# Kernel tuning notes

Hardware: AMD Instinct MI355X
Metric: run time of the kernel (lower is better)

## Reference

```python
import jax, jax.numpy as jnp
import numpy as np

# Straight-through sign binarization: forward -> {-1, +1}, backward -> identity
@jax.custom_vjp
def binarize(x):
    return jnp.where(x >= 0, jnp.ones_like(x), -jnp.ones_like(x))

def _bin_fwd(x):
    return binarize(x), None

def _bin_bwd(res, g):
    return (g,)

binarize.defvjp(_bin_fwd, _bin_bwd)

BATCH = 16384
IN_SIZE = 1025   # must be 2**n + 1
HIDDEN = 1025    # must be 2**n + 1

def setup_inputs() -> dict:
    key = jax.random.key(0)
    k0, k1, k2, k3 = jax.random.split(key, 4)
    # weight init scale per reset_parameters: sqrt(1.5/(in+out)) uniform
    s = float(np.sqrt(1.5 / (IN_SIZE + HIDDEN)))
    return {
        "x": jax.random.normal(k0, (BATCH, IN_SIZE), dtype=jnp.float32),
        "W0": jax.random.uniform(k1, (HIDDEN, IN_SIZE), jnp.float32, -s, s),
        "W1": jax.random.uniform(k2, (HIDDEN, HIDDEN), jnp.float32, -s, s),
        "W2": jax.random.uniform(k3, (1, HIDDEN), jnp.float32, -s, s),
    }

def reference(x, W0, W1, W2):
    # x: [B, IN_SIZE]; weights stored [out, in] (nn.Linear convention), no bias
    h = x.reshape(-1, IN_SIZE)
    for W in (W0, W1, W2):
        lin = h @ binarize(W).T          # float GEMM against +/-1 weights
        h = binarize(lin)                # sign activation
    # num_classes == 2 path: to_boolean maps {-1,+1} -> {0,1}, then squeeze
    out = (h + 1.0) * 0.5
    return out.squeeze(-1)               # [B]
```

## Files before the change

### kernel.cpp

```cpp
#include <hip/hip_runtime.h>
#include <cstdint>

typedef unsigned long long u64;
typedef unsigned short ushort_t;
typedef __attribute__((ext_vector_type(8))) short short8;
typedef __attribute__((ext_vector_type(4))) float f32x4;

#define B_TOTAL 16384
#define K_DIM   1025
#define O_DIM   1025
#define NWORDS  17
#define NKT     34
#define NFRAG   72
#define A_BYTES 8192
#define B_BYTES 73728
#define SMEM_BYTES 99328
#define FLAG_CAP 4096
#define L23_ROWS 16

__device__ __forceinline__ ushort_t f2bf_rne(float f) {
  unsigned u = __float_as_uint(f);
  return (ushort_t)((u + 0x7fffu + ((u >> 16) & 1u)) >> 16);
}

__global__ __launch_bounds__(256) void pack_all_kernel(const float* __restrict__ W0,
                                                       const float* __restrict__ W1,
                                                       const float* __restrict__ W2,
                                                       u64* __restrict__ w0b,
                                                       u64* __restrict__ w1b,
                                                       u64* __restrict__ w2b) {
  __shared__ unsigned char by[136];
  const int row = blockIdx.x, t = threadIdx.x;
  const float* src; u64* dst; int o;
  if (row < O_DIM)           { src = W0; dst = w0b; o = row; }
  else if (row < 2 * O_DIM)  { src = W1; dst = w1b; o = row - O_DIM; }
  else                       { src = W2; dst = w2b; o = 0; }
  if (t < 136) {
    const float* wr = src + (size_t)o * K_DIM;
    unsigned m = 0;
#pragma unroll
    for (int j = 0; j < 8; ++j) {
      int k = t * 8 + j;
      bool pos = (k < K_DIM) ? (wr[k] >= 0.0f) : true;
      m |= (unsigned)pos << j;
    }
    by[t] = (unsigned char)m;
  }
  __syncthreads();
  if (t < NWORDS) {
    u64 word = 0;
#pragma unroll
    for (int q = 0; q < 8; ++q) word |= (u64)by[t * 8 + q] << (8 * q);
    dst[(size_t)o * NWORDS + t] = word;
  }
}

__global__ __launch_bounds__(256) void prep_sbf_kernel(const float* __restrict__ w0,
                                                       ushort_t* __restrict__ sbf) {
  const int t = threadIdx.x;
  const int f = blockIdx.x * 4 + (t >> 6);
  const int lane = t & 63;
  const int kt = f / NFRAG, nf = f % NFRAG;
  const int o = nf * 16 + (lane & 15);
  const int kbase = kt * 32 + (lane >> 4) * 8;
  short8 sv;
#pragma unroll
  for (int j = 0; j < 8; ++j) {
    int k = kbase + j;
    short v = 0;
    if (o < O_DIM && k < K_DIM)
      v = (short)((w0[(size_t)o * K_DIM + k] >= 0.0f) ? 0x3F80 : 0xBF80);
    sv[j] = v;
  }
  *(short8*)&sbf[(size_t)f * 512 + lane * 8] = sv;
}

__global__ __launch_bounds__(512, 1) void l1_fused_kernel(
    const ushort_t* __restrict__ sbf, const float* __restrict__ x,
    const u64* __restrict__ w0b, u64* __restrict__ h1b) {
  extern __shared__ char smem[];
  const int p = blockIdx.x;
  const int t = threadIdx.x;
  const int wave = t >> 6, lane = t & 63;
  const int lr = lane & 15, lg = lane >> 4;
  const int b0 = p * 64;
  const int obase = wave * 144;

  const int u = t & 255;
  const int cmf = u >> 6, clane = u & 63;
  const int crow = cmf * 16 + (clane & 15);
  const int ckb0 = (clane >> 4) * 8;
  const bool isLo = (t >= 256);
  const float* xrowC = x + (size_t)(b0 + crow) * K_DIM;
  const int convOff = (isLo ? 4096 : 0) + cmf * 1024 + clane * 16;

  const ushort_t* gB = sbf + (size_t)(wave * 9) * 512 + lane * 8;

  f32x4 acc[4][9];
#pragma unroll
  for (int mf = 0; mf < 4; ++mf)
#pragma unroll
    for (int nfl = 0; nfl < 9; ++nfl)
#pragma unroll
      for (int c = 0; c < 4; ++c) acc[mf][nfl][c] = 0.0f;

  float xv[8];
  float sAcc = 0.0f;
  short8 bX[9];

#define LOADX(KT)                                                              \
  {                                                                            \
    int kb = (KT) * 32 + ckb0;                                                 \
    const float* xr = xrowC + kb;                                              \
    if (kb + 8 <= K_DIM) {                                                     \
      float4 a = *(const float4*)xr;                                           \
      float4 b = *(const float4*)(xr + 4);                                     \
      xv[0]=a.x; xv[1]=a.y; xv[2]=a.z; xv[3]=a.w;                              \
      xv[4]=b.x; xv[5]=b.y; xv[6]=b.z; xv[7]=b.w;                              \
    } else {                                                                   \
      _Pragma("unroll")                                                        \
      for (int j = 0; j < 8; ++j) xv[j] = (kb + j < K_DIM) ? xr[j] : 0.0f;     \
    }                                                                          \
  }

#define CONVERT_WRITE(DBUF)                                                    \
  {                                                                            \
    short8 w8;                                                                 \
    if (!isLo) {                                                               \
      _Pragma("unroll")                                                        \
      for (int j = 0; j < 8; ++j) {                                            \
        float v = xv[j];                                                       \
        sAcc += fabsf(v);                                                      \
        w8[j] = (short)f2bf_rne(v);                                            \
      }                                                                        \
    } else {                                                                   \
      _Pragma("unroll")                                                        \
      for (int j = 0; j < 8; ++j) {                                            \
        float v = xv[j];                                                       \
        ushort_t h = f2bf_rne(v);                                              \
        float hf = __uint_as_float((unsigned)h << 16);                         \
        w8[j] = (short)f2bf_rne(v - hf);                                       \
      }                                                                        \
    }                                                                          \
    *(short8*)((DBUF) + convOff) = w8;                                         \
  }

#define LOADB(KT)                                                              \
  {                                                                            \
    _Pragma("unroll")                                                          \
    for (int i = 0; i < 9; ++i)                                                \
      bX[i] = *(const short8*)&gB[(size_t)(KT) * (B_BYTES / 2) + i * 512];     \
  }

#define MFMA_STEP(AOFF, KTN)                                                   \
  {                                                                            \
    const ushort_t* A = (const ushort_t*)(smem + (AOFF));                      \
    const ushort_t* gBn = gB + (size_t)(KTN) * (B_BYTES / 2);                  \
    short8 ah[4], al[4];                                                       \
    _Pragma("unroll")                                                          \
    for (int mf = 0; mf < 4; ++mf) {                                           \
      ah[mf] = *(const short8*)&A[mf * 512 + lane * 8];                        \
      al[mf] = *(const short8*)&A[(4 + mf) * 512 + lane * 8];                  \
    }                                                                          \
    _Pragma("unroll")                                                          \
    for (int nfl = 0; nfl < 9; ++nfl) {                                        \
      short8 bv = bX[nfl];                                                     \
      bX[nfl] = *(const short8*)&gBn[nfl * 512];                               \
      _Pragma("unroll")                                                        \
      for (int mf = 0; mf < 4; ++mf) {                                         \
        acc[mf][nfl] = __builtin_amdgcn_mfma_f32_16x16x32_bf16(ah[mf], bv, acc[mf][nfl], 0, 0, 0); \
        acc[mf][nfl] = __builtin_amdgcn_mfma_f32_16x16x32_bf16(al[mf], bv, acc[mf][nfl], 0, 0, 0); \
      }                                                                        \
    }                                                                          \
  }

#define LDS_BARRIER()                                                          \
  {                                                                            \
    asm volatile("s_waitcnt lgkmcnt(0)" ::: "memory");                         \
    __builtin_amdgcn_s_barrier();                                              \
  }

  LOADX(0); CONVERT_WRITE(smem);
  LOADB(0);
  LOADX(1);
  LDS_BARRIER();

  for (int kt = 0; kt < NKT; kt += 2) {
    {
      CONVERT_WRITE(smem + 8192);
      if (kt + 2 < NKT) LOADX(kt + 2);
      MFMA_STEP(0, kt + 1);
      LDS_BARRIER();
    }
    {
      if (kt + 2 < NKT) CONVERT_WRITE(smem);
      if (kt + 3 < NKT) LOADX(kt + 3);
      const int ktn = (kt + 2 < NKT) ? (kt + 2) : (NKT - 1);
      MFMA_STEP(8192, ktn);
      LDS_BARRIER();
    }
  }
#undef LOADX
#undef CONVERT_WRITE
#undef LOADB
#undef MFMA_STEP
#undef LDS_BARRIER

  __syncthreads();

  unsigned char* bits = (unsigned char*)smem;
  u64*      hs    = (u64*)(smem + 73728);
  unsigned* list  = (unsigned*)(smem + 82432);
  unsigned* lcnt  = (unsigned*)(smem + 98816);
  float*    errbL = (float*)(smem + 98832);
  unsigned* hsw   = (unsigned*)hs;

  sAcc += __shfl_xor(sAcc, 16, 64);
  sAcc += __shfl_xor(sAcc, 32, 64);
  if (t == 0) *lcnt = 0;
  if (!isLo && lg == 0)
    errbL[crow] = sAcc * (1.02f / 65536.0f) + 0.125f;
  __syncthreads();

  float eb[4][4];
#pragma unroll
  for (int mf = 0; mf < 4; ++mf)
#pragma unroll
    for (int rg = 0; rg < 4; ++rg) eb[mf][rg] = errbL[mf * 16 + lg * 4 + rg];

#pragma unroll
  for (int mf = 0; mf < 4; ++mf)
#pragma unroll
    for (int nfl = 0; nfl < 9; ++nfl)
#pragma unroll
      for (int rg = 0; rg < 4; ++rg) {
        int bl = mf * 16 + lg * 4 + rg;
        int o  = obase + nfl * 16 + lr;
        float lin = acc[mf][nfl][rg];
        unsigned abit = (lin >= 0.0f) ? 1u : 0u;
        bits[bl * 1152 + o] = (unsigned char)abit;
        if ((o < O_DIM) && (fabsf(lin) <= eb[mf][rg])) {
          unsigned idx = atomicAdd(lcnt, 1u);
          if (idx < FLAG_CAP)
            list[idx] = ((unsigned)bl << 12) | ((unsigned)o << 1) | abit;
        }
      }
  __syncthreads();

  for (int task = t; task < 64 * NWORDS; task += 512) {
    int row = task / NWORDS, w = task % NWORDS;
    u64 word = 0;
#pragma unroll
    for (int q = 0; q < 8; ++q) {
      u64 v = *(const u64*)&bits[row * 1152 + w * 64 + q * 8];
#pragma unroll
      for (int m = 0; m < 8; ++m)
        word |= ((v >> (8 * m)) & 1ull) << (q * 8 + m);
    }
    int rem = O_DIM - w * 64;
    if (rem < 64) word |= (~0ull << rem);
    hs[row * NWORDS + w] = word;
  }
  __syncthreads();

  {
    unsigned n = *lcnt; if (n > FLAG_CAP) n = FLAG_CAP;
    for (unsigned i = t; i < n; i += 512) {
      unsigned en = list[i];
      int bl = (int)(en >> 12), o = (int)((en >> 1) & 0x7ffu);
      unsigned abit = en & 1u;
      const float* xr = x + (size_t)(b0 + bl) * K_DIM;
      const u64* wr = w0b + (size_t)o * NWORDS;
      float a = 0.0f;
      for (int j = 0; j < 16; ++j) {
        u64 wd = wr[j];
#pragma unroll
        for (int m = 0; m < 64; ++m) {
          float v = xr[j * 64 + m];
          unsigned neg = ((unsigned)(wd >> m) & 1u) ^ 1u;
          a += __uint_as_float(__float_as_uint(v) ^ (neg << 31));
        }
      }
      {
        u64 wd = wr[16];
        float v = xr[1024];
        unsigned neg = ((unsigned)wd & 1u) ^ 1u;
        a += __uint_as_float(__float_as_uint(v) ^ (neg << 31));
      }
      unsigned nb = (a >= 0.0f) ? 1u : 0u;
      if (nb != abit)
        atomicXor(&hsw[bl * 34 + (o >> 5)], 1u << (o & 31));
    }
  }
  __syncthreads();

  for (int task = t; task < 64 * NWORDS; task += 512)
    h1b[(size_t)b0 * NWORDS + task] = hs[task];
}

__global__ __launch_bounds__(256) void l2l3_kernel(const u64* __restrict__ h1b,
                                                   const u64* __restrict__ w1b,
                                                   const u64* __restrict__ w2b,
                                                   float* __restrict__ out) {
  __shared__ u64 hs[L23_ROWS][NWORDS];
  __shared__ u64 h2[L23_ROWS][NWORDS];
  const int bt = blockIdx.x;
  const int t = threadIdx.x;
  for (int i = t; i < L23_ROWS * NWORDS; i += 256)
    hs[i / NWORDS][i % NWORDS] = h1b[(size_t)(bt * L23_ROWS + i / NWORDS) * NWORDS + i % NWORDS];
  __syncthreads();

  const int w = t >> 6, l = t & 63;
  for (int oc = w; oc < NWORDS; oc += 4) {
    int o = oc * 64 + l;
    bool valid = (o < O_DIM);
    int orow = valid ? o : (O_DIM - 1);
    u64 wb[NWORDS];
#pragma unroll
    for (int j = 0; j < NWORDS; ++j) wb[j] = w1b[(size_t)orow * NWORDS + j];
    for (int b = 0; b < L23_ROWS; b += 2) {
      int p0 = 0, p1 = 0;
#pragma unroll
      for (int j = 0; j < NWORDS; ++j) {
        p0 += __popcll(hs[b + 0][j] ^ wb[j]);
        p1 += __popcll(hs[b + 1][j] ^ wb[j]);
      }
      u64 m0 = __ballot(valid ? (K_DIM - 2 * p0 >= 0) : true);
      u64 m1 = __ballot(valid ? (K_DIM - 2 * p1 >= 0) : true);
      if (l == 0) h2[b + 0][oc] = m0;
      if (l == 1) h2[b + 1][oc] = m1;
    }
  }
  __syncthreads();
  if (t < L23_ROWS) {
    int p = 0;
#pragma unroll
    for (int j = 0; j < NWORDS; ++j) p += __popcll(h2[t][j] ^ w2b[j]);
    out[bt * L23_ROWS + t] = ((K_DIM - 2 * p) >= 0) ? 1.0f : 0.0f;
  }
}

extern "C" void kernel_launch(void* const* d_in, const int* in_sizes, int n_in,
                              void* d_out, int out_size, void* d_ws, size_t ws_size,
                              hipStream_t stream) {
  const float* x  = (const float*)d_in[0];
  const float* W0 = (const float*)d_in[1];
  const float* W1 = (const float*)d_in[2];
  const float* W2 = (const float*)d_in[3];
  float* out = (float*)d_out;

  char* ws = (char*)d_ws;
  u64*      w0b  = (u64*)(ws);
  u64*      w1b  = (u64*)(ws + 139776);
  u64*      w2b  = (u64*)(ws + 279552);
  u64*      h1b  = (u64*)(ws + 280064);
  ushort_t* sbf  = (ushort_t*)(ws + 2508288);

  static bool attr_set = false;
  if (!attr_set) {
    hipFuncSetAttribute((const void*)l1_fused_kernel,
                        hipFuncAttributeMaxDynamicSharedMemorySize, SMEM_BYTES);
    attr_set = true;
  }

  pack_all_kernel<<<2 * O_DIM + 1, 256, 0, stream>>>(W0, W1, W2, w0b, w1b, w2b);
  prep_sbf_kernel<<<NKT * NFRAG / 4, 256, 0, stream>>>(W0, sbf);
  l1_fused_kernel<<<B_TOTAL / 64, 512, SMEM_BYTES, stream>>>(sbf, x, w0b, h1b);
  l2l3_kernel<<<B_TOTAL / L23_ROWS, 256, 0, stream>>>(h1b, w1b, w2b, out);
}
```

Measured before the change: 150.9 us.

## Split layer-1 GEMM N dimension across 12 waves with fewer fragments per wave

```diff
diff --git a/kernel.cpp b/kernel.cpp
--- a/kernel.cpp
+++ b/kernel.cpp
@@ -14,6 +14,8 @@
 #define NFRAG   72
 #define A_BYTES 8192
 #define B_BYTES 73728
+#define NT      768
+#define WFRAG   6
 #define SMEM_BYTES 99328
 #define FLAG_CAP 4096
 #define L23_ROWS 16
@@ -75,7 +77,7 @@
   *(short8*)&sbf[(size_t)f * 512 + lane * 8] = sv;
 }
 
-__global__ __launch_bounds__(512, 1) void l1_fused_kernel(
+__global__ __launch_bounds__(NT, 3) void l1_fused_kernel(
     const ushort_t* __restrict__ sbf, const float* __restrict__ x,
     const u64* __restrict__ w0b, u64* __restrict__ h1b) {
   extern __shared__ char smem[];
@@ -84,32 +86,33 @@
   const int wave = t >> 6, lane = t & 63;
   const int lr = lane & 15, lg = lane >> 4;
   const int b0 = p * 64;
-  const int obase = wave * 144;
+  const int obase = wave * (WFRAG * 16);
 
   const int u = t & 255;
   const int cmf = u >> 6, clane = u & 63;
   const int crow = cmf * 16 + (clane & 15);
   const int ckb0 = (clane >> 4) * 8;
-  const bool isLo = (t >= 256);
+  const bool isHi = (t < 256);
+  const bool doConv = (t < 512);
   const float* xrowC = x + (size_t)(b0 + crow) * K_DIM;
-  const int convOff = (isLo ? 4096 : 0) + cmf * 1024 + clane * 16;
-
-  const ushort_t* gB = sbf + (size_t)(wave * 9) * 512 + lane * 8;
-
-  f32x4 acc[4][9];
+  const int convOff = ((t >= 256) ? 4096 : 0) + cmf * 1024 + clane * 16;
+
+  const ushort_t* gB = sbf + (size_t)(wave * WFRAG) * 512 + lane * 8;
+
+  f32x4 acc[4][WFRAG];
 #pragma unroll
   for (int mf = 0; mf < 4; ++mf)
 #pragma unroll
-    for (int nfl = 0; nfl < 9; ++nfl)
+    for (int nfl = 0; nfl < WFRAG; ++nfl)
 #pragma unroll
       for (int c = 0; c < 4; ++c) acc[mf][nfl][c] = 0.0f;
 
   float xv[8];
   float sAcc = 0.0f;
-  short8 bX[9];
+  short8 bX[WFRAG];
 
 #define LOADX(KT)                                                              \
-  {                                                                            \
+  if (doConv) {                                                                \
     int kb = (KT) * 32 + ckb0;                                                 \
     const float* xr = xrowC + kb;                                              \
     if (kb + 8 <= K_DIM) {                                                     \
@@ -124,9 +127,9 @@
   }
 
 #define CONVERT_WRITE(DBUF)                                                    \
-  {                                                                            \
+  if (doConv) {                                                                \
     short8 w8;                                                                 \
-    if (!isLo) {                                                               \
+    if (isHi) {                                                                \
       _Pragma("unroll")                                                        \
       for (int j = 0; j < 8; ++j) {                                            \
         float v = xv[j];                                                       \
@@ -148,7 +151,7 @@
 #define LOADB(KT)                                                              \
   {                                                                            \
     _Pragma("unroll")                                                          \
-    for (int i = 0; i < 9; ++i)                                                \
+    for (int i = 0; i < WFRAG; ++i)                                            \
       bX[i] = *(const short8*)&gB[(size_t)(KT) * (B_BYTES / 2) + i * 512];     \
   }
 
@@ -163,7 +166,7 @@
       al[mf] = *(const short8*)&A[(4 + mf) * 512 + lane * 8];                  \
     }                                                                          \
     _Pragma("unroll")                                                          \
-    for (int nfl = 0; nfl < 9; ++nfl) {                                        \
+    for (int nfl = 0; nfl < WFRAG; ++nfl) {                                    \
       short8 bv = bX[nfl];                                                     \
       bX[nfl] = *(const short8*)&gBn[nfl * 512];                               \
       _Pragma("unroll")                                                        \
@@ -218,7 +221,7 @@
   sAcc += __shfl_xor(sAcc, 16, 64);
   sAcc += __shfl_xor(sAcc, 32, 64);
   if (t == 0) *lcnt = 0;
-  if (!isLo && lg == 0)
+  if (isHi && lg == 0)
     errbL[crow] = sAcc * (1.02f / 65536.0f) + 0.125f;
   __syncthreads();
 
@@ -231,7 +234,7 @@
 #pragma unroll
   for (int mf = 0; mf < 4; ++mf)
 #pragma unroll
-    for (int nfl = 0; nfl < 9; ++nfl)
+    for (int nfl = 0; nfl < WFRAG; ++nfl)
 #pragma unroll
       for (int rg = 0; rg < 4; ++rg) {
         int bl = mf * 16 + lg * 4 + rg;
@@ -247,7 +250,7 @@
       }
   __syncthreads();
 
-  for (int task = t; task < 64 * NWORDS; task += 512) {
+  for (int task = t; task < 64 * NWORDS; task += NT) {
     int row = task / NWORDS, w = task % NWORDS;
     u64 word = 0;
 #pragma unroll
@@ -265,7 +268,7 @@
 
   {
     unsigned n = *lcnt; if (n > FLAG_CAP) n = FLAG_CAP;
-    for (unsigned i = t; i < n; i += 512) {
+    for (unsigned i = t; i < n; i += NT) {
       unsigned en = list[i];
       int bl = (int)(en >> 12), o = (int)((en >> 1) & 0x7ffu);
       unsigned abit = en & 1u;
@@ -294,7 +297,7 @@
   }
   __syncthreads();
 
-  for (int task = t; task < 64 * NWORDS; task += 512)
+  for (int task = t; task < 64 * NWORDS; task += NT)
     h1b[(size_t)b0 * NWORDS + task] = hs[task];
 }
 
@@ -365,6 +368,6 @@
 
   pack_all_kernel<<<2 * O_DIM + 1, 256, 0, stream>>>(W0, W1, W2, w0b, w1b, w2b);
   prep_sbf_kernel<<<NKT * NFRAG / 4, 256, 0, stream>>>(W0, sbf);
-  l1_fused_kernel<<<B_TOTAL / 64, 512, SMEM_BYTES, stream>>>(sbf, x, w0b, h1b);
+  l1_fused_kernel<<<B_TOTAL / 64, NT, SMEM_BYTES, stream>>>(sbf, x, w0b, h1b);
   l2l3_kernel<<<B_TOTAL / L23_ROWS, 256, 0, stream>>>(h1b, w1b, w2b, out);
 }
```

New measurement: 166.1 us. +10.1%, slower.

## Double-buffer two k-tiles per stage to halve LDS barriers in GEMM loop

Applied to the files above, without the earlier changes.

```diff
diff --git a/kernel.cpp b/kernel.cpp
--- a/kernel.cpp
+++ b/kernel.cpp
@@ -104,39 +104,39 @@
 #pragma unroll
       for (int c = 0; c < 4; ++c) acc[mf][nfl][c] = 0.0f;
 
-  float xv[8];
+  float xvA[8], xvB[8];
   float sAcc = 0.0f;
   short8 bX[9];
 
-#define LOADX(KT)                                                              \
+#define LOADX(KT, XV)                                                          \
   {                                                                            \
     int kb = (KT) * 32 + ckb0;                                                 \
     const float* xr = xrowC + kb;                                              \
     if (kb + 8 <= K_DIM) {                                                     \
       float4 a = *(const float4*)xr;                                           \
       float4 b = *(const float4*)(xr + 4);                                     \
-      xv[0]=a.x; xv[1]=a.y; xv[2]=a.z; xv[3]=a.w;                              \
-      xv[4]=b.x; xv[5]=b.y; xv[6]=b.z; xv[7]=b.w;                              \
+      (XV)[0]=a.x; (XV)[1]=a.y; (XV)[2]=a.z; (XV)[3]=a.w;                      \
+      (XV)[4]=b.x; (XV)[5]=b.y; (XV)[6]=b.z; (XV)[7]=b.w;                      \
     } else {                                                                   \
       _Pragma("unroll")                                                        \
-      for (int j = 0; j < 8; ++j) xv[j] = (kb + j < K_DIM) ? xr[j] : 0.0f;     \
+      for (int j = 0; j < 8; ++j) (XV)[j] = (kb + j < K_DIM) ? xr[j] : 0.0f;   \
     }                                                                          \
   }
 
-#define CONVERT_WRITE(DBUF)                                                    \
+#define CONVERT_WRITE(DBUF, XV)                                                \
   {                                                                            \
     short8 w8;                                                                 \
     if (!isLo) {                                                               \
       _Pragma("unroll")                                                        \
       for (int j = 0; j < 8; ++j) {                                            \
-        float v = xv[j];                                                       \
+        float v = (XV)[j];                                                     \
         sAcc += fabsf(v);                                                      \
         w8[j] = (short)f2bf_rne(v);                                            \
       }                                                                        \
     } else {                                                                   \
       _Pragma("unroll")                                                        \
       for (int j = 0; j < 8; ++j) {                                            \
-        float v = xv[j];                                                       \
+        float v = (XV)[j];                                                     \
         ushort_t h = f2bf_rne(v);                                              \
         float hf = __uint_as_float((unsigned)h << 16);                         \
         w8[j] = (short)f2bf_rne(v - hf);                                       \
@@ -180,25 +180,28 @@
     __builtin_amdgcn_s_barrier();                                              \
   }
 
-  LOADX(0); CONVERT_WRITE(smem);
+  LOADX(0, xvA); LOADX(1, xvB);
+  CONVERT_WRITE(smem, xvA);
+  CONVERT_WRITE(smem + 8192, xvB);
   LOADB(0);
-  LOADX(1);
+  LOADX(2, xvA); LOADX(3, xvB);
   LDS_BARRIER();
 
+  int cur = 0;
   for (int kt = 0; kt < NKT; kt += 2) {
+    const int rd = cur * 16384;
+    const int wr = (cur ^ 1) * 16384;
+    if (kt + 2 < NKT) CONVERT_WRITE(smem + wr, xvA);
+    if (kt + 3 < NKT) CONVERT_WRITE(smem + wr + 8192, xvB);
+    if (kt + 4 < NKT) LOADX(kt + 4, xvA);
+    if (kt + 5 < NKT) LOADX(kt + 5, xvB);
+    MFMA_STEP(rd, kt + 1);
     {
-      CONVERT_WRITE(smem + 8192);
-      if (kt + 2 < NKT) LOADX(kt + 2);
-      MFMA_STEP(0, kt + 1);
-      LDS_BARRIER();
-    }
-    {
-      if (kt + 2 < NKT) CONVERT_WRITE(smem);
-      if (kt + 3 < NKT) LOADX(kt + 3);
       const int ktn = (kt + 2 < NKT) ? (kt + 2) : (NKT - 1);
-      MFMA_STEP(8192, ktn);
-      LDS_BARRIER();
-    }
+      MFMA_STEP(rd + 8192, ktn);
+    }
+    LDS_BARRIER();
+    cur ^= 1;
   }
 #undef LOADX
 #undef CONVERT_WRITE
```

After: 162.6 us. 1.08x slower.
